# Optimization experiments

Hardware: AMD Instinct MI355X
Metric: run time of the kernel (lower is better)

## Reference

```python
import jax, jax.numpy as jnp
import numpy as np

C = 256

def setup_inputs() -> dict:
    key = jax.random.key(0)
    ks = jax.random.split(key, 8)
    B, H, W = 4, 64, 64
    x = jax.random.normal(ks[0], (B, C, H, W), dtype=jnp.float32)
    # 1x1 conv weights ~ kaiming uniform; bias zero
    bound = np.sqrt(6.0 / C)
    Wq = jax.random.uniform(ks[1], (C, C), minval=-bound, maxval=bound, dtype=jnp.float32)
    Wk = jax.random.uniform(ks[2], (C, C), minval=-bound, maxval=bound, dtype=jnp.float32)
    Wv = jax.random.uniform(ks[3], (C, C), minval=-bound, maxval=bound, dtype=jnp.float32)
    bq = jnp.zeros((C,), jnp.float32)
    bk = jnp.zeros((C,), jnp.float32)
    bv = jnp.zeros((C,), jnp.float32)
    # gamma initialized to zero in torch; use small nonzero so output depends on attn path
    gamma = jnp.array([0.1], dtype=jnp.float32)
    return {"x": x, "Wq": Wq, "bq": bq, "Wk": Wk, "bk": bk, "Wv": Wv, "bv": bv, "gamma": gamma}


def reference(x, Wq, bq, Wk, bk, Wv, bv, gamma):
    B, Cc, H, W = x.shape
    N = H * W
    xf = x.reshape(B, Cc, N)  # [B,C,N]
    # 1x1 conv == per-pixel linear over channels: out[b,o,n] = sum_c W[o,c]*x[b,c,n] + b[o]
    q = jnp.einsum('oc,bcn->bon', Wq, xf) + bq[None, :, None]  # [B,C,N]
    k = jnp.einsum('oc,bcn->bon', Wk, xf) + bk[None, :, None]
    v = jnp.einsum('oc,bcn->bon', Wv, xf) + bv[None, :, None]
    # energy[b,i,j] = q[b,:,i] . k[b,:,j]  (no scaling, as in source)
    energy = jnp.einsum('bci,bcj->bij', q, k)  # [B,N,N]
    attention = jax.nn.softmax(energy, axis=-1)
    # out[b,c,i] = sum_j v[b,c,j] * attention[b,i,j]  (bmm(value, attn^T))
    out = jnp.einsum('bcj,bij->bci', v, attention)
    out = out.reshape(B, Cc, H, W)
    return gamma * out + x
```

## Files before the change

kernel.cpp:

```cpp
#include <hip/hip_runtime.h>
#include <hip/hip_bf16.h>
#include <cstdint>


#define C_DIM 256
#define N_DIM 4096
#define B_DIM 4

typedef _Float16 f16;
typedef f16 f16x8 __attribute__((ext_vector_type(8)));
typedef f16 f16x4 __attribute__((ext_vector_type(4)));
typedef float f32x4 __attribute__((ext_vector_type(4)));

__device__ __forceinline__ void dma16(const f16* g, f16* l) {
  __builtin_amdgcn_global_load_lds(
      (const __attribute__((address_space(1))) unsigned int*)g,
      (__attribute__((address_space(3))) unsigned int*)l, 16, 0, 0);
}

__global__ __launch_bounds__(256) void k_prep_xs(const float* __restrict__ x,
                                                 f16* __restrict__ xs) {
  __shared__ float tile[64][65];
  const int b = blockIdx.z, nb = blockIdx.x * 64, cb = blockIdx.y * 64;
  const float* xb = x + (size_t)b * C_DIM * N_DIM;
  for (int i = threadIdx.x; i < 64 * 64; i += 256) {
    int c = i >> 6, n = i & 63;
    tile[c][n] = xb[(size_t)(cb + c) * N_DIM + nb + n];
  }
  __syncthreads();
  f16* xsb = xs + (size_t)b * N_DIM * C_DIM;
  for (int i = threadIdx.x; i < 64 * 64; i += 256) {
    int n = i >> 6, c = i & 63;
    xsb[(size_t)(nb + n) * C_DIM + cb + c] = (f16)tile[c][n];
  }
}

__global__ __launch_bounds__(256) void k_cast_w(const float* __restrict__ Wq,
                                                const float* __restrict__ Wk,
                                                const float* __restrict__ Wv,
                                                f16* __restrict__ Wh) {
  int i = blockIdx.x * 256 + threadIdx.x;
  int sel = i >> 16, j = i & 65535;
  const float* s = (sel == 0) ? Wq : (sel == 1) ? Wk : Wv;
  Wh[i] = (f16)s[j];
}

__global__ __launch_bounds__(256) void k_proj(const f16* __restrict__ xs,
                                              const f16* __restrict__ Wh,
                                              const float* __restrict__ bq,
                                              const float* __restrict__ bk,
                                              const float* __restrict__ bv,
                                              f16* __restrict__ Qh,
                                              f16* __restrict__ Kh,
                                              f16* __restrict__ Vh) {
  const int z = blockIdx.y;
  const int w = threadIdx.x >> 6, lane = threadIdx.x & 63;
  const int quad = lane >> 4, li = lane & 15;
  const f16* W = Wh + (size_t)z * 65536;
  const float* bias = (z == 0) ? bq : (z == 1) ? bk : bv;

  if (z < 2) {
    f16* out = (z == 0) ? Qh : Kh;
    const int g0 = (blockIdx.x * 4 + w) * 16;
    f16x8 a[8];
    const f16* arow = xs + (size_t)(g0 + li) * C_DIM + quad * 8;
#pragma unroll
    for (int kf = 0; kf < 8; kf++) a[kf] = *(const f16x8*)(arow + kf * 32);
    for (int ot = 0; ot < 16; ot++) {
      f32x4 acc = {0.f, 0.f, 0.f, 0.f};
      const f16* brow = W + (size_t)(ot * 16 + li) * C_DIM + quad * 8;
#pragma unroll
      for (int kf = 0; kf < 8; kf++) {
        f16x8 bf = *(const f16x8*)(brow + kf * 32);
        acc = __builtin_amdgcn_mfma_f32_16x16x32_f16(a[kf], bf, acc, 0, 0, 0);
      }
      float bb = bias[ot * 16 + li];
      f16* orow = out + (size_t)g0 * C_DIM + ot * 16 + li;
#pragma unroll
      for (int r = 0; r < 4; r++)
        orow[(size_t)(quad * 4 + r) * C_DIM] = (f16)(acc[r] + bb);
    }
  } else {
    const int t = blockIdx.x * 4 + w;
    const int b = t >> 8, j0 = (t & 255) * 16;
    f16x8 bfr[8];
    const f16* brow = xs + (size_t)(b * N_DIM + j0 + li) * C_DIM + quad * 8;
#pragma unroll
    for (int kf = 0; kf < 8; kf++) bfr[kf] = *(const f16x8*)(brow + kf * 32);
    for (int ot = 0; ot < 16; ot++) {
      f32x4 acc = {0.f, 0.f, 0.f, 0.f};
      const f16* arow = W + (size_t)(ot * 16 + li) * C_DIM + quad * 8;
#pragma unroll
      for (int kf = 0; kf < 8; kf++) {
        f16x8 af = *(const f16x8*)(arow + kf * 32);
        acc = __builtin_amdgcn_mfma_f32_16x16x32_f16(af, bfr[kf], acc, 0, 0, 0);
      }
      f16* obase = Vh + ((size_t)(b * C_DIM + ot * 16 + quad * 4)) * N_DIM + j0 + li;
#pragma unroll
      for (int r = 0; r < 4; r++) {
        float bb = bias[ot * 16 + quad * 4 + r];
        obase[(size_t)r * N_DIM] = (f16)(acc[r] + bb);
      }
    }
  }
}

#define JT 64
#define NT (N_DIM / JT)
#define K0_OFF 0
#define K1_OFF 16384
#define V0_OFF 32768
#define V1_OFF 49152
#define P_OFF  65536
#define PSTR 40
#define SMEM_F16 70656
#define MRG_WSTR 4160
#define MRG_CSTR 260
#define ML_OFF   16640

__global__ __launch_bounds__(512, 1) void k_attn(const f16* __restrict__ Qh,
                                                 const f16* __restrict__ Kh,
                                                 const f16* __restrict__ Vh,
                                                 const float* __restrict__ x,
                                                 const float* __restrict__ gamma_p,
                                                 float* __restrict__ out) {
  __shared__ __align__(16) f16 smem[SMEM_F16];
  const int b = blockIdx.y;
  const int tid = threadIdx.x;
  const int w = tid >> 6, lane = tid & 63;
  const int wq = w & 3, wj = w >> 2;
  const int quad = lane >> 4, li = lane & 15;
  const int lw = li & 7;
  const int ibase = blockIdx.x * 64 + wq * 16;

  int ksl[8];
#pragma unroll
  for (int kf = 0; kf < 8; kf++) ksl[kf] = ((kf * 4 + quad) ^ lw) << 3;
  const int vsl = ((wj * 4 + quad) ^ lw) << 3;

  f16x8 qf[8];
  {
    const f16* qrow = Qh + (size_t)(b * N_DIM + ibase + li) * C_DIM + quad * 8;
#pragma unroll
    for (int kf = 0; kf < 8; kf++) qf[kf] = *(const f16x8*)(qrow + kf * 32);
  }
  const f16* Kb = Kh + (size_t)b * N_DIM * C_DIM;
  const f16* Vb = Vh + (size_t)b * C_DIM * N_DIM;
  f16* Pw = smem + P_OFF + w * 16 * PSTR;

  const float LOG2E = 1.4426950408889634f;
  float m = -3.0e38f, l = 0.0f;
  f32x4 acc[16];
#pragma unroll
  for (int ct = 0; ct < 16; ct++) acc[ct] = (f32x4){0.f, 0.f, 0.f, 0.f};

  {
#pragma unroll
    for (int it = 0; it < 4; it++) {
      int p = w * 4 + it;
      int krsw = (2 * it + (lane >> 5)) & 7;
      dma16(Kb + (size_t)(2 * p + (lane >> 5)) * C_DIM + (((lane & 31) ^ krsw) * 8),
            smem + K0_OFF + p * 512);
      dma16(Vb + (size_t)(p * 8 + (lane >> 3)) * N_DIM + (((lane & 7) ^ (lane >> 3)) * 8),
            smem + V0_OFF + p * 512);
    }
  }
  __syncthreads();

  for (int t = 0; t < NT; t++) {
    const f16* Kc = smem + ((t & 1) ? K1_OFF : K0_OFF);
    const f16* Vc = smem + ((t & 1) ? V1_OFF : V0_OFF);

    if (t + 1 < NT) {
      f16* Kn = smem + ((t & 1) ? K0_OFF : K1_OFF);
      f16* Vn = smem + ((t & 1) ? V0_OFF : V1_OFF);
      const int jt = (t + 1) * JT;
      const f16* kg = Kb + (size_t)jt * C_DIM;
      const f16* vg = Vb + jt;
#pragma unroll
      for (int it = 0; it < 4; it++) {
        int p = w * 4 + it;
        int krsw = (2 * it + (lane >> 5)) & 7;
        dma16(kg + (size_t)(2 * p + (lane >> 5)) * C_DIM + (((lane & 31) ^ krsw) * 8),
              Kn + p * 512);
        dma16(vg + (size_t)(p * 8 + (lane >> 3)) * N_DIM + (((lane & 7) ^ (lane >> 3)) * 8),
              Vn + p * 512);
      }
    }

    f32x4 s[2];
#pragma unroll
    for (int sub = 0; sub < 2; sub++) {
      f32x4 ss = {0.f, 0.f, 0.f, 0.f};
      const f16* krow = Kc + (wj * 32 + sub * 16 + li) * 256;
#pragma unroll
      for (int kf = 0; kf < 8; kf++) {
        f16x8 kfr = *(const f16x8*)(krow + ksl[kf]);
        ss = __builtin_amdgcn_mfma_f32_16x16x32_f16(kfr, qf[kf], ss, 0, 0, 0);
      }
      s[sub] = ss;
    }

    float tm = fmaxf(fmaxf(fmaxf(s[0][0], s[0][1]), fmaxf(s[0][2], s[0][3])),
                     fmaxf(fmaxf(s[1][0], s[1][1]), fmaxf(s[1][2], s[1][3])));
    tm = fmaxf(tm, __shfl_xor(tm, 16));
    tm = fmaxf(tm, __shfl_xor(tm, 32));
    float nm = fmaxf(m, tm);
    float alpha = exp2f((m - nm) * LOG2E);
    m = nm;
    if (__any(alpha < 1.0f)) {
      l *= alpha;
#pragma unroll
      for (int ct = 0; ct < 16; ct++) {
        acc[ct][0] *= alpha; acc[ct][1] *= alpha;
        acc[ct][2] *= alpha; acc[ct][3] *= alpha;
      }
    }
#pragma unroll
    for (int sub = 0; sub < 2; sub++) {
      float p0 = exp2f((s[sub][0] - m) * LOG2E);
      float p1 = exp2f((s[sub][1] - m) * LOG2E);
      float p2 = exp2f((s[sub][2] - m) * LOG2E);
      float p3 = exp2f((s[sub][3] - m) * LOG2E);
      l += (p0 + p1) + (p2 + p3);
      *(f16x4*)(Pw + li * PSTR + sub * 16 + quad * 4) =
          (f16x4){(f16)p0, (f16)p1, (f16)p2, (f16)p3};
    }

    f16x8 pf = *(const f16x8*)(Pw + li * PSTR + quad * 8);
#pragma unroll
    for (int ct = 0; ct < 16; ct++) {
      const f16* vrow = Vc + (ct * 16 + li) * 64;
      f16x8 v = *(const f16x8*)(vrow + vsl);
      acc[ct] = __builtin_amdgcn_mfma_f32_16x16x32_f16(v, pf, acc[ct], 0, 0, 0);
    }

    __syncthreads();
  }

  l += __shfl_xor(l, 16);
  l += __shfl_xor(l, 32);

  float* mrg = (float*)smem;
  if (wj == 1) {
    const int u = wq;
    float* base = mrg + u * MRG_WSTR + li * MRG_CSTR;
#pragma unroll
    for (int ct = 0; ct < 16; ct++)
      *(f32x4*)(base + ct * 16 + quad * 4) = acc[ct];
    if (lane < 16) {
      mrg[ML_OFF + u * 32 + li] = m;
      mrg[ML_OFF + u * 32 + 16 + li] = l;
    }
  }
  __syncthreads();
  if (wj == 0) {
    const int u = wq;
    const float m_b = mrg[ML_OFF + u * 32 + li];
    const float l_b = mrg[ML_OFF + u * 32 + 16 + li];
    const float M = fmaxf(m, m_b);
    const float aa = exp2f((m - M) * LOG2E);
    const float ab = exp2f((m_b - M) * LOG2E);
    const float lm = aa * l + ab * l_b;
    const float scale = gamma_p[0] / lm;
    const float* base = mrg + u * MRG_WSTR + li * MRG_CSTR;

    const float* xb = x + (size_t)b * C_DIM * N_DIM;
    float* ob = out + (size_t)b * C_DIM * N_DIM;
    const int icol = ibase + li;
#pragma unroll
    for (int ct = 0; ct < 16; ct++) {
      f32x4 accb = *(const f32x4*)(base + ct * 16 + quad * 4);
#pragma unroll
      for (int r = 0; r < 4; r++) {
        size_t off = (size_t)(ct * 16 + quad * 4 + r) * N_DIM + icol;
        ob[off] = (acc[ct][r] * aa + accb[r] * ab) * scale + xb[off];
      }
    }
  }
}

extern "C" void kernel_launch(void* const* d_in, const int* in_sizes, int n_in,
                              void* d_out, int out_size, void* d_ws, size_t ws_size,
                              hipStream_t stream) {
  const float* x     = (const float*)d_in[0];
  const float* Wq    = (const float*)d_in[1];
  const float* bq    = (const float*)d_in[2];
  const float* Wk    = (const float*)d_in[3];
  const float* bk    = (const float*)d_in[4];
  const float* Wv    = (const float*)d_in[5];
  const float* bv    = (const float*)d_in[6];
  const float* gamma = (const float*)d_in[7];
  float* out = (float*)d_out;

  char* ws = (char*)d_ws;
  f16* xs = (f16*)(ws);
  f16* Qh = (f16*)(ws + (size_t)8  * 1024 * 1024);
  f16* Kh = (f16*)(ws + (size_t)16 * 1024 * 1024);
  f16* Vh = (f16*)(ws + (size_t)24 * 1024 * 1024);
  f16* Wh = (f16*)(ws + (size_t)32 * 1024 * 1024);

  k_prep_xs<<<dim3(64, 4, 4), 256, 0, stream>>>(x, xs);
  k_cast_w<<<dim3(768), 256, 0, stream>>>(Wq, Wk, Wv, Wh);
  k_proj<<<dim3(256, 3), 256, 0, stream>>>(xs, Wh, bq, bk, bv, Qh, Kh, Vh);
  k_attn<<<dim3(64, 4), 512, 0, stream>>>(Qh, Kh, Vh, x, gamma, out);
}
```

Before: 258.6 us.

## Fuse x transpose/cast into QKV projection kernel with shared-memory tile

Removes the separate transpose-and-cast kernel and the xs workspace: the new QKV kernel loads a 64-pixel tile of x, converts it to fp16 into swizzled shared memory, and computes Q, K and V from that tile. Each block reuses the shared x fragments across all three projections. Outputs are written as vectorized f16x4 stores. This cuts one launch and a full read/write of an intermediate buffer. The cost is a 256-block grid, far fewer blocks than before, and strided global reads of x during the tile load.

```diff
diff --git a/kernel.cpp b/kernel.cpp
--- a/kernel.cpp
+++ b/kernel.cpp
@@ -16,23 +16,6 @@
   __builtin_amdgcn_global_load_lds(
       (const __attribute__((address_space(1))) unsigned int*)g,
       (__attribute__((address_space(3))) unsigned int*)l, 16, 0, 0);
-}
-
-__global__ __launch_bounds__(256) void k_prep_xs(const float* __restrict__ x,
-                                                 f16* __restrict__ xs) {
-  __shared__ float tile[64][65];
-  const int b = blockIdx.z, nb = blockIdx.x * 64, cb = blockIdx.y * 64;
-  const float* xb = x + (size_t)b * C_DIM * N_DIM;
-  for (int i = threadIdx.x; i < 64 * 64; i += 256) {
-    int c = i >> 6, n = i & 63;
-    tile[c][n] = xb[(size_t)(cb + c) * N_DIM + nb + n];
-  }
-  __syncthreads();
-  f16* xsb = xs + (size_t)b * N_DIM * C_DIM;
-  for (int i = threadIdx.x; i < 64 * 64; i += 256) {
-    int n = i >> 6, c = i & 63;
-    xsb[(size_t)(nb + n) * C_DIM + cb + c] = (f16)tile[c][n];
-  }
 }
 
 __global__ __launch_bounds__(256) void k_cast_w(const float* __restrict__ Wq,
@@ -45,62 +28,85 @@
   Wh[i] = (f16)s[j];
 }
 
-__global__ __launch_bounds__(256) void k_proj(const f16* __restrict__ xs,
-                                              const f16* __restrict__ Wh,
-                                              const float* __restrict__ bq,
-                                              const float* __restrict__ bk,
-                                              const float* __restrict__ bv,
-                                              f16* __restrict__ Qh,
-                                              f16* __restrict__ Kh,
-                                              f16* __restrict__ Vh) {
-  const int z = blockIdx.y;
-  const int w = threadIdx.x >> 6, lane = threadIdx.x & 63;
+__global__ __launch_bounds__(512) void k_qkv(const float* __restrict__ x,
+                                             const f16* __restrict__ Wh,
+                                             const float* __restrict__ bq,
+                                             const float* __restrict__ bk,
+                                             const float* __restrict__ bv,
+                                             f16* __restrict__ Qh,
+                                             f16* __restrict__ Kh,
+                                             f16* __restrict__ Vh) {
+  __shared__ __align__(16) f16 xt[64 * 256];
+  const int b = blockIdx.y, n0 = blockIdx.x * 64;
+  const int tid = threadIdx.x;
+  const int w = tid >> 6, lane = tid & 63;
   const int quad = lane >> 4, li = lane & 15;
-  const f16* W = Wh + (size_t)z * 65536;
-  const float* bias = (z == 0) ? bq : (z == 1) ? bk : bv;
-
-  if (z < 2) {
-    f16* out = (z == 0) ? Qh : Kh;
-    const int g0 = (blockIdx.x * 4 + w) * 16;
-    f16x8 a[8];
-    const f16* arow = xs + (size_t)(g0 + li) * C_DIM + quad * 8;
-#pragma unroll
-    for (int kf = 0; kf < 8; kf++) a[kf] = *(const f16x8*)(arow + kf * 32);
+  const int gt = w & 3, role = w >> 2;
+
+  {
+    const float* xb = x + (size_t)b * C_DIM * N_DIM + n0;
+#pragma unroll
+    for (int cg = 0; cg < 4; cg++) {
+      f16x8 v;
+#pragma unroll
+      for (int j = 0; j < 8; j++) {
+        int c = w * 32 + cg * 8 + j;
+        v[j] = (f16)xb[(size_t)c * N_DIM + lane];
+      }
+      int chunk = w * 4 + cg;
+      int slot = chunk ^ (lane & 7);
+      *(f16x8*)(&xt[lane * 256 + slot * 8]) = v;
+    }
+  }
+  __syncthreads();
+
+  int xsl[8];
+#pragma unroll
+  for (int kf = 0; kf < 8; kf++) xsl[kf] = ((kf * 4 + quad) ^ (li & 7)) << 3;
+  f16x8 xf[8];
+  {
+    const f16* xrow = xt + (gt * 16 + li) * 256;
+#pragma unroll
+    for (int kf = 0; kf < 8; kf++) xf[kf] = *(const f16x8*)(xrow + xsl[kf]);
+  }
+
+  {
+    const f16* W = Wh + (size_t)role * 65536;
+    const float* bias = role ? bk : bq;
+    f16* out = role ? Kh : Qh;
+    const size_t grow = (size_t)(b * N_DIM + n0 + gt * 16 + li) * C_DIM;
     for (int ot = 0; ot < 16; ot++) {
       f32x4 acc = {0.f, 0.f, 0.f, 0.f};
-      const f16* brow = W + (size_t)(ot * 16 + li) * C_DIM + quad * 8;
+      const f16* wrow = W + (size_t)(ot * 16 + li) * C_DIM + quad * 8;
 #pragma unroll
       for (int kf = 0; kf < 8; kf++) {
-        f16x8 bf = *(const f16x8*)(brow + kf * 32);
-        acc = __builtin_amdgcn_mfma_f32_16x16x32_f16(a[kf], bf, acc, 0, 0, 0);
-      }
-      float bb = bias[ot * 16 + li];
-      f16* orow = out + (size_t)g0 * C_DIM + ot * 16 + li;
-#pragma unroll
-      for (int r = 0; r < 4; r++)
-        orow[(size_t)(quad * 4 + r) * C_DIM] = (f16)(acc[r] + bb);
-    }
-  } else {
-    const int t = blockIdx.x * 4 + w;
-    const int b = t >> 8, j0 = (t & 255) * 16;
-    f16x8 bfr[8];
-    const f16* brow = xs + (size_t)(b * N_DIM + j0 + li) * C_DIM + quad * 8;
-#pragma unroll
-    for (int kf = 0; kf < 8; kf++) bfr[kf] = *(const f16x8*)(brow + kf * 32);
-    for (int ot = 0; ot < 16; ot++) {
+        f16x8 wf = *(const f16x8*)(wrow + kf * 32);
+        acc = __builtin_amdgcn_mfma_f32_16x16x32_f16(wf, xf[kf], acc, 0, 0, 0);
+      }
+      const int o0 = ot * 16 + quad * 4;
+      f16x4 st = {(f16)(acc[0] + bias[o0]), (f16)(acc[1] + bias[o0 + 1]),
+                  (f16)(acc[2] + bias[o0 + 2]), (f16)(acc[3] + bias[o0 + 3])};
+      *(f16x4*)(out + grow + o0) = st;
+    }
+  }
+
+  {
+    const f16* W = Wh + (size_t)2 * 65536;
+#pragma unroll
+    for (int ot8 = 0; ot8 < 8; ot8++) {
+      const int ot = role * 8 + ot8;
       f32x4 acc = {0.f, 0.f, 0.f, 0.f};
-      const f16* arow = W + (size_t)(ot * 16 + li) * C_DIM + quad * 8;
+      const f16* wrow = W + (size_t)(ot * 16 + li) * C_DIM + quad * 8;
 #pragma unroll
       for (int kf = 0; kf < 8; kf++) {
-        f16x8 af = *(const f16x8*)(arow + kf * 32);
-        acc = __builtin_amdgcn_mfma_f32_16x16x32_f16(af, bfr[kf], acc, 0, 0, 0);
-      }
-      f16* obase = Vh + ((size_t)(b * C_DIM + ot * 16 + quad * 4)) * N_DIM + j0 + li;
-#pragma unroll
-      for (int r = 0; r < 4; r++) {
-        float bb = bias[ot * 16 + quad * 4 + r];
-        obase[(size_t)r * N_DIM] = (f16)(acc[r] + bb);
-      }
+        f16x8 wf = *(const f16x8*)(wrow + kf * 32);
+        acc = __builtin_amdgcn_mfma_f32_16x16x32_f16(xf[kf], wf, acc, 0, 0, 0);
+      }
+      const float bb = bv[ot * 16 + li];
+      f16x4 st = {(f16)(acc[0] + bb), (f16)(acc[1] + bb),
+                  (f16)(acc[2] + bb), (f16)(acc[3] + bb)};
+      *(f16x4*)(Vh + (size_t)(b * C_DIM + ot * 16 + li) * N_DIM +
+                n0 + gt * 16 + quad * 4) = st;
     }
   }
 }
@@ -294,14 +300,12 @@
   float* out = (float*)d_out;
 
   char* ws = (char*)d_ws;
-  f16* xs = (f16*)(ws);
-  f16* Qh = (f16*)(ws + (size_t)8  * 1024 * 1024);
-  f16* Kh = (f16*)(ws + (size_t)16 * 1024 * 1024);
-  f16* Vh = (f16*)(ws + (size_t)24 * 1024 * 1024);
-  f16* Wh = (f16*)(ws + (size_t)32 * 1024 * 1024);
-
-  k_prep_xs<<<dim3(64, 4, 4), 256, 0, stream>>>(x, xs);
+  f16* Qh = (f16*)(ws);
+  f16* Kh = (f16*)(ws + (size_t)8  * 1024 * 1024);
+  f16* Vh = (f16*)(ws + (size_t)16 * 1024 * 1024);
+  f16* Wh = (f16*)(ws + (size_t)24 * 1024 * 1024);
+
   k_cast_w<<<dim3(768), 256, 0, stream>>>(Wq, Wk, Wv, Wh);
-  k_proj<<<dim3(256, 3), 256, 0, stream>>>(xs, Wh, bq, bk, bv, Qh, Kh, Vh);
+  k_qkv<<<dim3(64, 4), 512, 0, stream>>>(x, Wh, bq, bk, bv, Qh, Kh, Vh);
   k_attn<<<dim3(64, 4), 512, 0, stream>>>(Qh, Kh, Vh, x, gamma, out);
 }
```

After: 250.2 us, median of 2. -3.2%, faster.
